# Optimization experiments

Hardware: AMD Instinct MI355X
Metric: run time of the kernel (lower is better)

## Reference

```python
import jax, jax.numpy as jnp
import numpy as np

H = 16
D = 64
EPS = 1e-6

def _phi(x):
    # elu_feature_map: elu(x) + 1
    return jax.nn.elu(x) + 1.0

def setup_inputs() -> dict:
    key = jax.random.key(0)
    k1, k2, k3, k4 = jax.random.split(key, 4)
    B, N = 4, 4096
    query = jax.random.normal(k1, (B, N, H * D), dtype=jnp.float32)
    key_t = jax.random.normal(k2, (B, N, H * D), dtype=jnp.float32)
    value = jax.random.normal(k3, (B, N, H * D), dtype=jnp.float32)
    W_out = jax.random.normal(k4, (D, H * D), dtype=jnp.float32) * (1.0 / np.sqrt(H * D))
    b_out = jnp.zeros((D,), dtype=jnp.float32)
    return {"query": query, "key": key_t, "value": value, "W_out": W_out, "b_out": b_out}

def reference(query, key, value, W_out, b_out):
    B, N, _ = query.shape
    # b n (h d) -> b h n d
    def split_heads(x):
        return x.reshape(B, N, H, D).transpose(0, 2, 1, 3)
    q = split_heads(query)
    k = split_heads(key)
    v = split_heads(value)
    Q = _phi(q)  # [B,H,N,D]
    K = _phi(k)
    # KV aggregation: O(N D^2)
    KV = jnp.einsum('bhnd,bhnm->bhdm', K, v)          # [B,H,D,D]
    Ksum = K.sum(axis=2)                               # [B,H,D]
    Z = 1.0 / (jnp.einsum('bhnd,bhd->bhn', Q, Ksum) + EPS)  # [B,H,N]
    out = jnp.einsum('bhnd,bhdm,bhn->bhnm', Q, KV, Z)  # [B,H,N,D]
    # b h n d -> b n h d -> (b*n, h*d)
    out = out.transpose(0, 2, 1, 3).reshape(B * N, H * D)
    return out @ W_out.T + b_out
```

## Files before the change

### kernel.cpp

```cpp
#include <hip/hip_runtime.h>

#define B_  4
#define N_  4096
#define H_  16
#define D_  64
#define BH_ 64
#define S_  8
#define HS_ 4
#define EPS_ 1e-6f

typedef _Float16 h2  __attribute__((ext_vector_type(2)));
typedef float    f4v __attribute__((ext_vector_type(4)));

struct H2x4 { h2 e[4]; };

__device__ __forceinline__ H2x4 ld_h2x4(const h2* p) {
    f4v r = *(const f4v*)p;
    return __builtin_bit_cast(H2x4, r);
}

__device__ __forceinline__ float phi(float x) {
    return x > 0.0f ? x + 1.0f : __expf(x);
}

__device__ __forceinline__ float fdot2(h2 a, h2 b, float c) {
    return __builtin_amdgcn_fdot2(a, b, c, false);
}

__global__ __launch_bounds__(256) void k_kvpart(const float* __restrict__ K,
                                                const float* __restrict__ V,
                                                float* __restrict__ kvpart,
                                                float* __restrict__ kspart) {
    const int bh = blockIdx.x;
    const int s  = blockIdx.y;
    const int b  = bh >> 4;
    const int h  = bh & 15;
    const int t  = threadIdx.x;
    const int w  = t >> 6;
    const int lane = t & 63;

    __shared__ __align__(16) float pool[2 * 64 * 68];
    __shared__ float ksred[4][64];

    h2* Kp = (h2*)pool;
    h2* Vp = (h2*)(pool + 2176);

    const int dbase = (lane >> 3) * 8;
    const int mbase = (lane & 7) * 8;

    float acc[8][8] = {{0.f}};
    float ksum[8]   = {0.f};
    h2 one2; one2.x = (_Float16)1.0f; one2.y = (_Float16)1.0f;

    const float4* Kf4 = (const float4*)K;
    const float4* Vf4 = (const float4*)V;

    for (int chunk = 0; chunk < (N_ / S_) / 64; ++chunk) {
        const int n0 = s * (N_ / S_) + chunk * 64;
        __syncthreads();
#pragma unroll
        for (int rep = 0; rep < 2; ++rep) {
            int idx = t + rep * 256;
            int rp = idx >> 4, c4 = idx & 15;
            size_t g = (size_t)(b * N_ + n0 + 2 * rp) * 256 + h * 16 + c4;
            float4 a = Kf4[g];
            float4 c = Kf4[g + 256];
            H2x4 o;
            o.e[0].x = (_Float16)phi(a.x); o.e[0].y = (_Float16)phi(c.x);
            o.e[1].x = (_Float16)phi(a.y); o.e[1].y = (_Float16)phi(c.y);
            o.e[2].x = (_Float16)phi(a.z); o.e[2].y = (_Float16)phi(c.z);
            o.e[3].x = (_Float16)phi(a.w); o.e[3].y = (_Float16)phi(c.w);
            *(f4v*)&Kp[rp * 68 + c4 * 4] = __builtin_bit_cast(f4v, o);
        }
#pragma unroll
        for (int rep = 0; rep < 2; ++rep) {
            int idx = t + rep * 256;
            int rp = idx >> 4, c4 = idx & 15;
            size_t g = (size_t)(b * N_ + n0 + 2 * rp) * 256 + h * 16 + c4;
            float4 a = Vf4[g];
            float4 c = Vf4[g + 256];
            H2x4 o;
            o.e[0].x = (_Float16)a.x; o.e[0].y = (_Float16)c.x;
            o.e[1].x = (_Float16)a.y; o.e[1].y = (_Float16)c.y;
            o.e[2].x = (_Float16)a.z; o.e[2].y = (_Float16)c.z;
            o.e[3].x = (_Float16)a.w; o.e[3].y = (_Float16)c.w;
            *(f4v*)&Vp[rp * 68 + c4 * 4] = __builtin_bit_cast(f4v, o);
        }
        __syncthreads();
#pragma unroll
        for (int cc = 0; cc < 8; ++cc) {
            int c = w * 8 + cc;
            H2x4 kd0 = ld_h2x4(&Kp[c * 68 + dbase]);
            H2x4 kd1 = ld_h2x4(&Kp[c * 68 + dbase + 4]);
            H2x4 vm0 = ld_h2x4(&Vp[c * 68 + mbase]);
            H2x4 vm1 = ld_h2x4(&Vp[c * 68 + mbase + 4]);
            h2 kd[8] = {kd0.e[0], kd0.e[1], kd0.e[2], kd0.e[3],
                        kd1.e[0], kd1.e[1], kd1.e[2], kd1.e[3]};
            h2 vm[8] = {vm0.e[0], vm0.e[1], vm0.e[2], vm0.e[3],
                        vm1.e[0], vm1.e[1], vm1.e[2], vm1.e[3]};
#pragma unroll
            for (int i = 0; i < 8; ++i) {
#pragma unroll
                for (int j = 0; j < 8; ++j) acc[i][j] = fdot2(kd[i], vm[j], acc[i][j]);
                ksum[i] = fdot2(kd[i], one2, ksum[i]);
            }
        }
    }

    if ((lane & 7) == 0) {
#pragma unroll
        for (int i = 0; i < 8; ++i) ksred[w][dbase + i] = ksum[i];
    }
    float* Red = pool;
    __syncthreads();

#define WRITE_T(slot)                                                          \
    {   float* T = Red + (slot) * 64 * 68;                                     \
        _Pragma("unroll")                                                      \
        for (int i = 0; i < 8; ++i) {                                          \
            f4v o0 = {acc[i][0], acc[i][1], acc[i][2], acc[i][3]};             \
            f4v o1 = {acc[i][4], acc[i][5], acc[i][6], acc[i][7]};             \
            *(f4v*)&T[(dbase + i) * 68 + mbase]     = o0;                      \
            *(f4v*)&T[(dbase + i) * 68 + mbase + 4] = o1;                      \
        } }
#define ADD_T(slot)                                                            \
    {   float* T = Red + (slot) * 64 * 68;                                     \
        _Pragma("unroll")                                                      \
        for (int i = 0; i < 8; ++i) {                                          \
            f4v r0 = *(f4v*)&T[(dbase + i) * 68 + mbase];                      \
            f4v r1 = *(f4v*)&T[(dbase + i) * 68 + mbase + 4];                  \
            acc[i][0] += r0[0]; acc[i][1] += r0[1];                            \
            acc[i][2] += r0[2]; acc[i][3] += r0[3];                            \
            acc[i][4] += r1[0]; acc[i][5] += r1[1];                            \
            acc[i][6] += r1[2]; acc[i][7] += r1[3];                            \
        } }

    if (w == 1) WRITE_T(0);
    if (w == 3) WRITE_T(1);
    __syncthreads();
    if (w == 0) ADD_T(0);
    if (w == 2) ADD_T(1);
    __syncthreads();
    if (w == 2) WRITE_T(0);
    __syncthreads();
    if (w == 0) {
        ADD_T(0);
        float4* kvp4 = (float4*)kvpart;
        const size_t base = (size_t)(bh * S_ + s) * 4096;
#pragma unroll
        for (int i = 0; i < 8; ++i) {
            float4 o0 = make_float4(acc[i][0], acc[i][1], acc[i][2], acc[i][3]);
            float4 o1 = make_float4(acc[i][4], acc[i][5], acc[i][6], acc[i][7]);
            kvp4[(base + (size_t)(dbase + i) * 64 + mbase) / 4]     = o0;
            kvp4[(base + (size_t)(dbase + i) * 64 + mbase + 4) / 4] = o1;
        }
        float ks = ksred[0][lane] + ksred[1][lane] + ksred[2][lane] + ksred[3][lane];
        kspart[(size_t)(bh * S_ + s) * 64 + lane] = ks;
    }
#undef WRITE_T
#undef ADD_T
}

__global__ __launch_bounds__(256) void k_makeM(const float* __restrict__ kvpart,
                                               const float* __restrict__ kspart,
                                               const float* __restrict__ W,
                                               float* __restrict__ Mh,
                                               float* __restrict__ Ksum) {
    const int bh = blockIdx.x;
    const int h  = bh & 15;
    const int t  = threadIdx.x;

    __shared__ float KVs[64][68];
    __shared__ float Ws[64][68];

    const float4* kv4 = (const float4*)kvpart;
    const float4* W4  = (const float4*)W;

    for (int idx = t; idx < 1024; idx += 256) {
        int row = idx >> 4, c4 = idx & 15;
        float4 r = make_float4(0.f, 0.f, 0.f, 0.f);
        for (int s = 0; s < S_; ++s) {
            float4 a = kv4[(size_t)(bh * S_ + s) * 1024 + idx];
            r.x += a.x; r.y += a.y; r.z += a.z; r.w += a.w;
        }
        *(float4*)&KVs[row][c4 * 4] = r;
        *(float4*)&Ws[row][c4 * 4] = W4[(size_t)row * 256 + h * 16 + c4];
    }
    if (t < 64) {
        float ks = 0.f;
        for (int s = 0; s < S_; ++s) ks += kspart[(size_t)(bh * S_ + s) * 64 + t];
        Ksum[(size_t)bh * 64 + t] = ks;
    }
    __syncthreads();

    const int dbase = (t >> 4) * 4, jbase = (t & 15) * 4;
    float acc[4][4] = {{0.f}};
#pragma unroll 4
    for (int m4 = 0; m4 < 16; ++m4) {
        float4 kvr[4], wr[4];
#pragma unroll
        for (int i = 0; i < 4; ++i) kvr[i] = *(const float4*)&KVs[dbase + i][m4 * 4];
#pragma unroll
        for (int j = 0; j < 4; ++j) wr[j] = *(const float4*)&Ws[jbase + j][m4 * 4];
#pragma unroll
        for (int i = 0; i < 4; ++i)
#pragma unroll
            for (int j = 0; j < 4; ++j)
                acc[i][j] += kvr[i].x * wr[j].x + kvr[i].y * wr[j].y +
                             kvr[i].z * wr[j].z + kvr[i].w * wr[j].w;
    }
    f4v* M4 = (f4v*)Mh;
#pragma unroll
    for (int p = 0; p < 2; ++p) {
        int c = (dbase >> 1) + p;
        H2x4 o;
#pragma unroll
        for (int j = 0; j < 4; ++j) {
            o.e[j].x = (_Float16)acc[2 * p][j];
            o.e[j].y = (_Float16)acc[2 * p + 1][j];
        }
        M4[((size_t)bh * 2048 + c * 64 + jbase) / 4] = __builtin_bit_cast(f4v, o);
    }
}

__global__ __launch_bounds__(256) void k_out(const float* __restrict__ Q,
                                             const float* __restrict__ Mh,
                                             const float* __restrict__ Ksum,
                                             float* __restrict__ outpart) {
    const int nc = blockIdx.x;
    const int b  = blockIdx.y;
    const int hs = blockIdx.z;
    const int n0 = nc * 128;
    const int t  = threadIdx.x;

    __shared__ __align__(16) h2 QpT[32][132];
    __shared__ __align__(16) h2 Msp[32][68];
    __shared__ h2 Kssh[32];

    const int ibase = (t >> 4) * 8;
    const int jbase = (t & 15) * 4;
    float acc_out[8][4] = {{0.f}};

    const float4* Qf4 = (const float4*)Q;
    const f4v*    M4  = (const f4v*)Mh;

    for (int hh = 0; hh < 4; ++hh) {
        const int h  = hs * 4 + hh;
        const int bh = b * 16 + h;
        __syncthreads();
#pragma unroll
        for (int rep = 0; rep < 8; ++rep) {
            int idx = t + rep * 256;
            int row = idx >> 4, c4 = idx & 15;
            float4 qq = Qf4[(size_t)(b * N_ + n0 + row) * 256 + h * 16 + c4];
            h2 p0; p0.x = (_Float16)phi(qq.x); p0.y = (_Float16)phi(qq.y);
            h2 p1; p1.x = (_Float16)phi(qq.z); p1.y = (_Float16)phi(qq.w);
            QpT[2 * c4][row]     = p0;
            QpT[2 * c4 + 1][row] = p1;
        }
#pragma unroll
        for (int rep = 0; rep < 2; ++rep) {
            int i2 = t + rep * 256;
            int c = i2 >> 4, j4 = (i2 & 15) * 4;
            *(f4v*)&Msp[c][j4] = M4[(size_t)bh * 512 + i2];
        }
        if (t < 32) {
            h2 ks; ks.x = (_Float16)Ksum[(size_t)bh * 64 + 2 * t];
            ks.y = (_Float16)Ksum[(size_t)bh * 64 + 2 * t + 1];
            Kssh[t] = ks;
        }
        __syncthreads();

        float sacc[8][4] = {{0.f}};
        float zacc[8]    = {0.f};
#pragma unroll 4
        for (int c = 0; c < 32; ++c) {
            H2x4 qa = ld_h2x4(&QpT[c][ibase]);
            H2x4 qb = ld_h2x4(&QpT[c][ibase + 4]);
            H2x4 mm = ld_h2x4(&Msp[c][jbase]);
            h2 ks = Kssh[c];
            h2 q[8] = {qa.e[0], qa.e[1], qa.e[2], qa.e[3],
                       qb.e[0], qb.e[1], qb.e[2], qb.e[3]};
#pragma unroll
            for (int i = 0; i < 8; ++i) {
                zacc[i] = fdot2(q[i], ks, zacc[i]);
#pragma unroll
                for (int j = 0; j < 4; ++j) sacc[i][j] = fdot2(q[i], mm.e[j], sacc[i][j]);
            }
        }
#pragma unroll
        for (int i = 0; i < 8; ++i) {
            float z = 1.0f / (zacc[i] + EPS_);
#pragma unroll
            for (int j = 0; j < 4; ++j) acc_out[i][j] += z * sacc[i][j];
        }
    }

    float4* O4 = (float4*)outpart;
    const size_t slice = (size_t)hs * (B_ * N_ * 64);
#pragma unroll
    for (int i = 0; i < 8; ++i) {
        float4 o = make_float4(acc_out[i][0], acc_out[i][1], acc_out[i][2], acc_out[i][3]);
        O4[(slice + (size_t)(b * N_ + n0 + ibase + i) * 64 + jbase) / 4] = o;
    }
}

__global__ __launch_bounds__(256) void k_red(const float* __restrict__ outpart,
                                             const float* __restrict__ bout,
                                             float* __restrict__ out) {
    const int p = blockIdx.x * 256 + threadIdx.x;
    const float4* P4 = (const float4*)outpart;
    const float4* B4 = (const float4*)bout;
    float4 o = B4[p & 15];
    const int stride = B_ * N_ * 64 / 4;
#pragma unroll
    for (int hs = 0; hs < HS_; ++hs) {
        float4 a = P4[(size_t)hs * stride + p];
        o.x += a.x; o.y += a.y; o.z += a.z; o.w += a.w;
    }
    ((float4*)out)[p] = o;
}

extern "C" void kernel_launch(void* const* d_in, const int* in_sizes, int n_in,
                              void* d_out, int out_size, void* d_ws, size_t ws_size,
                              hipStream_t stream) {
    const float* q  = (const float*)d_in[0];
    const float* k  = (const float*)d_in[1];
    const float* v  = (const float*)d_in[2];
    const float* W  = (const float*)d_in[3];
    const float* bo = (const float*)d_in[4];
    float* out = (float*)d_out;

    float* ws      = (float*)d_ws;
    float* kvpart  = ws;
    float* kspart  = kvpart + (size_t)BH_ * S_ * 4096;
    float* Mh      = kspart + (size_t)BH_ * S_ * 64;
    float* Ksum    = Mh + (size_t)BH_ * 2048;
    float* outpart = Ksum + (size_t)BH_ * 64;

    k_kvpart<<<dim3(BH_, S_), 256, 0, stream>>>(k, v, kvpart, kspart);
    k_makeM<<<BH_, 256, 0, stream>>>(kvpart, kspart, W, Mh, Ksum);
    k_out<<<dim3(N_ / 128, B_, HS_), 256, 0, stream>>>(q, Mh, Ksum, outpart);
    k_red<<<B_ * N_ * 64 / 4 / 256, 256, 0, stream>>>(outpart, bo, out);
}
```

Baseline: 248.4 us.

## Double-buffer K/V and Q staging with register prefetch, doubling grid parallelism

Both the KV-aggregation kernel and the output kernel now load the next chunk (or head) from global memory into registers while the current one is computed from shared memory. Staging uses two shared-memory buffers, so each iteration needs one barrier instead of two. The KV split count goes from 8 to 16 and the output kernel tile shrinks from 128 to 64 rows, which doubles the block count in both kernels to fill more CUs. The cost is more registers for the prefetch buffers, more shared memory, and a larger kvpart workspace for the makeM reduction to read.

New measurement: 261.6 us. 1.05x slower.

```diff
diff --git a/kernel.cpp b/kernel.cpp
--- a/kernel.cpp
+++ b/kernel.cpp
@@ -5,7 +5,7 @@
 #define H_  16
 #define D_  64
 #define BH_ 64
-#define S_  8
+#define S_  16
 #define HS_ 4
 #define EPS_ 1e-6f
 
@@ -13,14 +13,22 @@
 typedef float    f4v __attribute__((ext_vector_type(4)));
 
 struct H2x4 { h2 e[4]; };
+struct H2x2 { h2 a, b; };
 
 __device__ __forceinline__ H2x4 ld_h2x4(const h2* p) {
     f4v r = *(const f4v*)p;
     return __builtin_bit_cast(H2x4, r);
 }
+__device__ __forceinline__ void st_h2x2(h2* p, h2 a, h2 b) {
+    H2x2 t{a, b};
+    *(float2*)p = __builtin_bit_cast(float2, t);
+}
 
 __device__ __forceinline__ float phi(float x) {
     return x > 0.0f ? x + 1.0f : __expf(x);
+}
+__device__ __forceinline__ h2 phi2(float x, float y) {
+    h2 r; r.x = (_Float16)phi(x); r.y = (_Float16)phi(y); return r;
 }
 
 __device__ __forceinline__ float fdot2(h2 a, h2 b, float c) {
@@ -38,12 +46,11 @@
     const int t  = threadIdx.x;
     const int w  = t >> 6;
     const int lane = t & 63;
-
-    __shared__ __align__(16) float pool[2 * 64 * 68];
+    const int rp = t >> 4;
+    const int c4 = t & 15;
+
+    __shared__ __align__(16) float pool[2 * 4352];
     __shared__ float ksred[4][64];
-
-    h2* Kp = (h2*)pool;
-    h2* Vp = (h2*)(pool + 2176);
 
     const int dbase = (lane >> 3) * 8;
     const int mbase = (lane & 7) * 8;
@@ -55,38 +62,48 @@
     const float4* Kf4 = (const float4*)K;
     const float4* Vf4 = (const float4*)V;
 
-    for (int chunk = 0; chunk < (N_ / S_) / 64; ++chunk) {
+    const int chunks = N_ / (S_ * 64);
+
+    float4 kreg[4], vreg[4];
+
+    auto LOAD = [&](int chunk) {
         const int n0 = s * (N_ / S_) + chunk * 64;
+        size_t g = (size_t)(b * N_ + n0 + 2 * rp) * 256 + h * 16 + c4;
+        kreg[0] = Kf4[g];             kreg[1] = Kf4[g + 256];
+        kreg[2] = Kf4[g + 32 * 256];  kreg[3] = Kf4[g + 33 * 256];
+        vreg[0] = Vf4[g];             vreg[1] = Vf4[g + 256];
+        vreg[2] = Vf4[g + 32 * 256];  vreg[3] = Vf4[g + 33 * 256];
+    };
+    auto STORE = [&](int buf) {
+        h2* Kp = (h2*)(pool + buf * 4352);
+        h2* Vp = (h2*)(pool + buf * 4352 + 2176);
+#pragma unroll
+        for (int rep = 0; rep < 2; ++rep) {
+            int rpx = rp + 16 * rep;
+            float4 a = kreg[2 * rep], c = kreg[2 * rep + 1];
+            H2x4 o;
+            o.e[0] = phi2(a.x, c.x); o.e[1] = phi2(a.y, c.y);
+            o.e[2] = phi2(a.z, c.z); o.e[3] = phi2(a.w, c.w);
+            *(f4v*)&Kp[rpx * 68 + c4 * 4] = __builtin_bit_cast(f4v, o);
+            a = vreg[2 * rep]; c = vreg[2 * rep + 1];
+            H2x4 p;
+            p.e[0].x = (_Float16)a.x; p.e[0].y = (_Float16)c.x;
+            p.e[1].x = (_Float16)a.y; p.e[1].y = (_Float16)c.y;
+            p.e[2].x = (_Float16)a.z; p.e[2].y = (_Float16)c.z;
+            p.e[3].x = (_Float16)a.w; p.e[3].y = (_Float16)c.w;
+            *(f4v*)&Vp[rpx * 68 + c4 * 4] = __builtin_bit_cast(f4v, p);
+        }
+    };
+
+    LOAD(0);
+    STORE(0);
+
+    for (int chunk = 0; chunk < chunks; ++chunk) {
+        if (chunk + 1 < chunks) LOAD(chunk + 1);
         __syncthreads();
-#pragma unroll
-        for (int rep = 0; rep < 2; ++rep) {
-            int idx = t + rep * 256;
-            int rp = idx >> 4, c4 = idx & 15;
-            size_t g = (size_t)(b * N_ + n0 + 2 * rp) * 256 + h * 16 + c4;
-            float4 a = Kf4[g];
-            float4 c = Kf4[g + 256];
-            H2x4 o;
-            o.e[0].x = (_Float16)phi(a.x); o.e[0].y = (_Float16)phi(c.x);
-            o.e[1].x = (_Float16)phi(a.y); o.e[1].y = (_Float16)phi(c.y);
-            o.e[2].x = (_Float16)phi(a.z); o.e[2].y = (_Float16)phi(c.z);
-            o.e[3].x = (_Float16)phi(a.w); o.e[3].y = (_Float16)phi(c.w);
-            *(f4v*)&Kp[rp * 68 + c4 * 4] = __builtin_bit_cast(f4v, o);
-        }
-#pragma unroll
-        for (int rep = 0; rep < 2; ++rep) {
-            int idx = t + rep * 256;
-            int rp = idx >> 4, c4 = idx & 15;
-            size_t g = (size_t)(b * N_ + n0 + 2 * rp) * 256 + h * 16 + c4;
-            float4 a = Vf4[g];
-            float4 c = Vf4[g + 256];
-            H2x4 o;
-            o.e[0].x = (_Float16)a.x; o.e[0].y = (_Float16)c.x;
-            o.e[1].x = (_Float16)a.y; o.e[1].y = (_Float16)c.y;
-            o.e[2].x = (_Float16)a.z; o.e[2].y = (_Float16)c.z;
-            o.e[3].x = (_Float16)a.w; o.e[3].y = (_Float16)c.w;
-            *(f4v*)&Vp[rp * 68 + c4 * 4] = __builtin_bit_cast(f4v, o);
-        }
-        __syncthreads();
+        const int buf = chunk & 1;
+        const h2* Kp = (const h2*)(pool + buf * 4352);
+        const h2* Vp = (const h2*)(pool + buf * 4352 + 2176);
 #pragma unroll
         for (int cc = 0; cc < 8; ++cc) {
             int c = w * 8 + cc;
@@ -105,6 +122,7 @@
                 ksum[i] = fdot2(kd[i], one2, ksum[i]);
             }
         }
+        if (chunk + 1 < chunks) STORE((chunk + 1) & 1);
     }
 
     if ((lane & 7) == 0) {
@@ -115,7 +133,7 @@
     __syncthreads();
 
 #define WRITE_T(slot)                                                          \
-    {   float* T = Red + (slot) * 64 * 68;                                     \
+    {   float* T = Red + (slot) * 4352;                                        \
         _Pragma("unroll")                                                      \
         for (int i = 0; i < 8; ++i) {                                          \
             f4v o0 = {acc[i][0], acc[i][1], acc[i][2], acc[i][3]};             \
@@ -124,7 +142,7 @@
             *(f4v*)&T[(dbase + i) * 68 + mbase + 4] = o1;                      \
         } }
 #define ADD_T(slot)                                                            \
-    {   float* T = Red + (slot) * 64 * 68;                                     \
+    {   float* T = Red + (slot) * 4352;                                        \
         _Pragma("unroll")                                                      \
         for (int i = 0; i < 8; ++i) {                                          \
             f4v r0 = *(f4v*)&T[(dbase + i) * 68 + mbase];                      \
@@ -179,6 +197,7 @@
     for (int idx = t; idx < 1024; idx += 256) {
         int row = idx >> 4, c4 = idx & 15;
         float4 r = make_float4(0.f, 0.f, 0.f, 0.f);
+#pragma unroll 4
         for (int s = 0; s < S_; ++s) {
             float4 a = kv4[(size_t)(bh * S_ + s) * 1024 + idx];
             r.x += a.x; r.y += a.y; r.z += a.z; r.w += a.w;
@@ -230,76 +249,87 @@
     const int nc = blockIdx.x;
     const int b  = blockIdx.y;
     const int hs = blockIdx.z;
-    const int n0 = nc * 128;
+    const int n0 = nc * 64;
     const int t  = threadIdx.x;
-
-    __shared__ __align__(16) h2 QpT[32][132];
-    __shared__ __align__(16) h2 Msp[32][68];
-    __shared__ h2 Kssh[32];
-
-    const int ibase = (t >> 4) * 8;
+    const int rp = t >> 4;
+    const int c4 = t & 15;
+
+    __shared__ __align__(16) h2 QpT[2][32 * 70];
+    __shared__ __align__(16) h2 Msp[2][32 * 72];
+    __shared__ h2 Kss[2][32];
+
+    const int ibase = (t >> 4) * 4;
     const int jbase = (t & 15) * 4;
-    float acc_out[8][4] = {{0.f}};
+    float acc_out[4][4] = {{0.f}};
 
     const float4* Qf4 = (const float4*)Q;
     const f4v*    M4  = (const f4v*)Mh;
 
-    for (int hh = 0; hh < 4; ++hh) {
+    float4 qr[4]; f4v mr[2]; float ksa = 0.f, ksb = 0.f;
+
+    auto LOAD = [&](int hh) {
         const int h  = hs * 4 + hh;
         const int bh = b * 16 + h;
+        size_t g = (size_t)(b * N_ + n0 + 2 * rp) * 256 + h * 16 + c4;
+        qr[0] = Qf4[g];            qr[1] = Qf4[g + 256];
+        qr[2] = Qf4[g + 32 * 256]; qr[3] = Qf4[g + 33 * 256];
+        mr[0] = M4[(size_t)bh * 512 + t];
+        mr[1] = M4[(size_t)bh * 512 + t + 256];
+        if (t < 32) {
+            ksa = Ksum[(size_t)bh * 64 + 2 * t];
+            ksb = Ksum[(size_t)bh * 64 + 2 * t + 1];
+        }
+    };
+    auto STOREH = [&](int buf) {
+#pragma unroll
+        for (int rep = 0; rep < 2; ++rep) {
+            int rpx = rp + 16 * rep;
+            float4 a = qr[2 * rep], c = qr[2 * rep + 1];
+            st_h2x2(&QpT[buf][(2 * c4) * 70 + 2 * rpx],
+                    phi2(a.x, a.y), phi2(c.x, c.y));
+            st_h2x2(&QpT[buf][(2 * c4 + 1) * 70 + 2 * rpx],
+                    phi2(a.z, a.w), phi2(c.z, c.w));
+        }
+        *(f4v*)&Msp[buf][(t >> 4) * 72 + (t & 15) * 4]        = mr[0];
+        *(f4v*)&Msp[buf][((t >> 4) + 16) * 72 + (t & 15) * 4] = mr[1];
+        if (t < 32) { h2 k; k.x = (_Float16)ksa; k.y = (_Float16)ksb; Kss[buf][t] = k; }
+    };
+
+    LOAD(0);
+    STOREH(0);
+
+    for (int hh = 0; hh < 4; ++hh) {
+        if (hh + 1 < 4) LOAD(hh + 1);
         __syncthreads();
-#pragma unroll
-        for (int rep = 0; rep < 8; ++rep) {
-            int idx = t + rep * 256;
-            int row = idx >> 4, c4 = idx & 15;
-            float4 qq = Qf4[(size_t)(b * N_ + n0 + row) * 256 + h * 16 + c4];
-            h2 p0; p0.x = (_Float16)phi(qq.x); p0.y = (_Float16)phi(qq.y);
-            h2 p1; p1.x = (_Float16)phi(qq.z); p1.y = (_Float16)phi(qq.w);
-            QpT[2 * c4][row]     = p0;
-            QpT[2 * c4 + 1][row] = p1;
-        }
-#pragma unroll
-        for (int rep = 0; rep < 2; ++rep) {
-            int i2 = t + rep * 256;
-            int c = i2 >> 4, j4 = (i2 & 15) * 4;
-            *(f4v*)&Msp[c][j4] = M4[(size_t)bh * 512 + i2];
-        }
-        if (t < 32) {
-            h2 ks; ks.x = (_Float16)Ksum[(size_t)bh * 64 + 2 * t];
-            ks.y = (_Float16)Ksum[(size_t)bh * 64 + 2 * t + 1];
-            Kssh[t] = ks;
-        }
-        __syncthreads();
-
-        float sacc[8][4] = {{0.f}};
-        float zacc[8]    = {0.f};
-#pragma unroll 4
+        const int buf = hh & 1;
+
+        float sacc[4][4] = {{0.f}};
+        float zacc[4]    = {0.f};
+#pragma unroll 8
         for (int c = 0; c < 32; ++c) {
-            H2x4 qa = ld_h2x4(&QpT[c][ibase]);
-            H2x4 qb = ld_h2x4(&QpT[c][ibase + 4]);
-            H2x4 mm = ld_h2x4(&Msp[c][jbase]);
-            h2 ks = Kssh[c];
-            h2 q[8] = {qa.e[0], qa.e[1], qa.e[2], qa.e[3],
-                       qb.e[0], qb.e[1], qb.e[2], qb.e[3]};
-#pragma unroll
-            for (int i = 0; i < 8; ++i) {
-                zacc[i] = fdot2(q[i], ks, zacc[i]);
-#pragma unroll
-                for (int j = 0; j < 4; ++j) sacc[i][j] = fdot2(q[i], mm.e[j], sacc[i][j]);
+            H2x4 q = ld_h2x4(&QpT[buf][c * 70 + ibase]);
+            H2x4 m = ld_h2x4(&Msp[buf][c * 72 + jbase]);
+            h2 ks = Kss[buf][c];
+#pragma unroll
+            for (int i = 0; i < 4; ++i) {
+                zacc[i] = fdot2(q.e[i], ks, zacc[i]);
+#pragma unroll
+                for (int j = 0; j < 4; ++j) sacc[i][j] = fdot2(q.e[i], m.e[j], sacc[i][j]);
             }
         }
 #pragma unroll
-        for (int i = 0; i < 8; ++i) {
+        for (int i = 0; i < 4; ++i) {
             float z = 1.0f / (zacc[i] + EPS_);
 #pragma unroll
             for (int j = 0; j < 4; ++j) acc_out[i][j] += z * sacc[i][j];
         }
+        if (hh + 1 < 4) STOREH((hh + 1) & 1);
     }
 
     float4* O4 = (float4*)outpart;
     const size_t slice = (size_t)hs * (B_ * N_ * 64);
 #pragma unroll
-    for (int i = 0; i < 8; ++i) {
+    for (int i = 0; i < 4; ++i) {
         float4 o = make_float4(acc_out[i][0], acc_out[i][1], acc_out[i][2], acc_out[i][3]);
         O4[(slice + (size_t)(b * N_ + n0 + ibase + i) * 64 + jbase) / 4] = o;
     }
@@ -340,6 +370,6 @@
 
     k_kvpart<<<dim3(BH_, S_), 256, 0, stream>>>(k, v, kvpart, kspart);
     k_makeM<<<BH_, 256, 0, stream>>>(kvpart, kspart, W, Mh, Ksum);
-    k_out<<<dim3(N_ / 128, B_, HS_), 256, 0, stream>>>(q, Mh, Ksum, outpart);
+    k_out<<<dim3(N_ / 64, B_, HS_), 256, 0, stream>>>(q, Mh, Ksum, outpart);
     k_red<<<B_ * N_ * 64 / 4 / 256, 256, 0, stream>>>(outpart, bo, out);
 }
```
